# Kernel optimization log

Hardware: AMD Instinct MI355X
Metric: run time of the kernel (lower is better)

The kernel has to match this reference:

```python
import jax, jax.numpy as jnp
import numpy as np

TOP_N = 10
N_HEADS = 8

def _layernorm(x, g, b, eps=1e-5):
    mu = jnp.mean(x, axis=-1, keepdims=True)
    var = jnp.mean((x - mu) ** 2, axis=-1, keepdims=True)
    return (x - mu) * jax.lax.rsqrt(var + eps) * g + b

def setup_inputs() -> dict:
    key = jax.random.key(0)
    ks = jax.random.split(key, 16)
    B, N, D = 4096, 32768, 512
    s = 1.0 / np.sqrt(D)
    inp = {
        "visit_rep": jax.random.normal(ks[0], (B, D), jnp.float32),
        "E_mem_patient_rep": jax.random.normal(ks[1], (N, D), jnp.float32),
        "E_mem_med_rep": jax.random.normal(ks[2], (N, D), jnp.float32),
        "Wq": jax.random.uniform(ks[3], (D, D), jnp.float32, -s, s),
        "Wk": jax.random.uniform(ks[4], (D, D), jnp.float32, -s, s),
        "Wv": jax.random.uniform(ks[5], (D, D), jnp.float32, -s, s),
        "bq": jnp.zeros((D,), jnp.float32),
        "bk": jnp.zeros((D,), jnp.float32),
        "bv": jnp.zeros((D,), jnp.float32),
        "Wo": jax.random.uniform(ks[6], (D, D), jnp.float32, -s, s),
        "bo": jnp.zeros((D,), jnp.float32),
        "W1": jax.random.uniform(ks[7], (D, D), jnp.float32, -s, s),
        "b1": jax.random.uniform(ks[8], (D,), jnp.float32, -s, s),
        "W2": jax.random.uniform(ks[9], (D, D), jnp.float32, -s, s),
        "b2": jax.random.uniform(ks[10], (D,), jnp.float32, -s, s),
        "ln1_g": jnp.ones((D,), jnp.float32),
        "ln1_b": jnp.zeros((D,), jnp.float32),
        "ln2_g": jnp.ones((D,), jnp.float32),
        "ln2_b": jnp.zeros((D,), jnp.float32),
    }
    return inp

def reference(visit_rep, E_mem_patient_rep, E_mem_med_rep,
              Wq, bq, Wk, bk, Wv, bv, Wo, bo,
              W1, b1, W2, b2, ln1_g, ln1_b, ln2_g, ln2_b):
    B, D = visit_rep.shape
    H = N_HEADS
    hd = D // H
    # --- exact L2 kNN (faiss GpuIndexFlatL2 equivalent), detached ---
    q = jax.lax.stop_gradient(visit_rep)
    M = jax.lax.stop_gradient(E_mem_patient_rep)
    d2 = (jnp.sum(q * q, axis=1, keepdims=True)
          - 2.0 * q @ M.T
          + jnp.sum(M * M, axis=1)[None, :])          # [B, N]
    _, I = jax.lax.top_k(-d2, TOP_N)                    # [B, top_n]
    k = E_mem_patient_rep[I]                            # [B, top_n, D]
    v = E_mem_med_rep[I]                                # [B, top_n, D]
    # --- multihead attention, query seq-len 1 ---
    qh = (visit_rep @ Wq.T + bq).reshape(B, H, hd)
    kh = (k @ Wk.T + bk).reshape(B, TOP_N, H, hd)
    vh = (v @ Wv.T + bv).reshape(B, TOP_N, H, hd)
    scores = jnp.einsum("bhd,bnhd->bhn", qh, kh) / np.sqrt(hd)
    attn = jax.nn.softmax(scores, axis=-1)
    ctx = jnp.einsum("bhn,bnhd->bhd", attn, vh).reshape(B, D)
    attn_out = ctx @ Wo.T + bo
    # --- residual + norms + FFN (dropout = identity in eval) ---
    x = _layernorm(visit_rep + attn_out, ln1_g, ln1_b)
    ff = (jax.nn.leaky_relu(x @ W1.T + b1, 0.01)) @ W2.T + b2
    x = _layernorm(x + ff, ln2_g, ln2_b)
    return x
```

## Files before the change

kernel.cpp:

```cpp
#include <hip/hip_runtime.h>
#include <math.h>

#define BQ 4096
#define NMEM 32768
#define DD 512
#define TOPN 10
#define NBX 128
#define ENT 2048
#define NCF 16
#define LK 6
#define FINF 3.402823466e+38f
#define IMAX 0x7fffffff

typedef __attribute__((ext_vector_type(8))) short    bf16x8;
typedef __attribute__((ext_vector_type(4))) float    f32x4;
typedef __attribute__((ext_vector_type(4))) int      i32x4;

__device__ __forceinline__ unsigned short f2bf(float x) {
    unsigned int u = __float_as_uint(x);
    u += 0x7fffu + ((u >> 16) & 1u);
    return (unsigned short)(u >> 16);
}
__device__ __forceinline__ void async_copy16(const void* gp, void* lp) {
    __builtin_amdgcn_global_load_lds(
        (const __attribute__((address_space(1))) void*)gp,
        (__attribute__((address_space(3))) void*)lp, 16, 0, 0);
}
__device__ __forceinline__ bool lt_si(float s, int j, float s2, int j2) {
    return (s < s2) || (s == s2 && j < j2);
}
template<int KN>
__device__ __forceinline__ void topk_insert(float (&ts)[KN], int (&ti)[KN], float s, int j) {
    if (!lt_si(s, j, ts[KN-1], ti[KN-1])) return;
    #pragma unroll
    for (int p = KN-1; p > 0; --p) {
        if (lt_si(s, j, ts[p-1], ti[p-1])) { ts[p] = ts[p-1]; ti[p] = ti[p-1]; }
        else { ts[p] = s; ti[p] = j; return; }
    }
    ts[0] = s; ti[0] = j;
}

struct CastDesc {
    const float* in[7];
    unsigned short* out[7];
    int start[8];
};
__global__ __launch_bounds__(256) void cast_multi_kernel(CastDesc d) {
    int blk = blockIdx.x;
    int seg = 0;
    #pragma unroll
    for (int s = 0; s < 6; ++s) seg += (blk >= d.start[s + 1]) ? 1 : 0;
    int local = blk - d.start[seg];
    int i = (local * 256 + threadIdx.x) * 4;
    float4 v = *(const float4*)(d.in[seg] + i);
    ushort4 o;
    o.x = f2bf(v.x); o.y = f2bf(v.y); o.z = f2bf(v.z); o.w = f2bf(v.w);
    *(ushort4*)(d.out[seg] + i) = o;
}

__global__ __launch_bounds__(256) void cast_norm2_kernel(
        const float* __restrict__ inA, unsigned short* __restrict__ outA,
        const float* __restrict__ inB, unsigned short* __restrict__ outB,
        const float* __restrict__ inV,
        signed char* __restrict__ outA8, signed char* __restrict__ outV8,
        float* __restrict__ mnorm, float* __restrict__ msc,
        float* __restrict__ qsc) {
    const int pl = blockIdx.y;
    if (pl == 2 && blockIdx.x >= BQ / 4) return;
    const float* in = (pl == 0) ? inA : (pl == 1 ? inB : inV);
    int row = blockIdx.x * 4 + (threadIdx.x >> 6);
    int lane = threadIdx.x & 63;
    const float* r = in + (size_t)row * DD + lane * 8;
    float4 a = *(const float4*)r;
    float4 b = *(const float4*)(r + 4);
    if (pl < 2) {
        unsigned short* out = pl ? outB : outA;
        ushort4 oa, ob;
        oa.x = f2bf(a.x); oa.y = f2bf(a.y); oa.z = f2bf(a.z); oa.w = f2bf(a.w);
        ob.x = f2bf(b.x); ob.y = f2bf(b.y); ob.z = f2bf(b.z); ob.w = f2bf(b.w);
        unsigned short* op = out + (size_t)row * DD + lane * 8;
        *(ushort4*)op = oa; *(ushort4*)(op + 4) = ob;
    }
    if (pl != 1) {
        float ax = fmaxf(fmaxf(fmaxf(fabsf(a.x), fabsf(a.y)), fmaxf(fabsf(a.z), fabsf(a.w))),
                         fmaxf(fmaxf(fabsf(b.x), fabsf(b.y)), fmaxf(fabsf(b.z), fabsf(b.w))));
        float s = a.x*a.x + a.y*a.y + a.z*a.z + a.w*a.w
                + b.x*b.x + b.y*b.y + b.z*b.z + b.w*b.w;
        #pragma unroll
        for (int off = 32; off; off >>= 1) {
            ax = fmaxf(ax, __shfl_xor(ax, off, 64));
            if (pl == 0) s += __shfl_xor(s, off, 64);
        }
        ax = fmaxf(ax, 1e-30f);
        float inv = 127.0f / ax;
        int q[8];
        q[0] = __float2int_rn(a.x*inv); q[1] = __float2int_rn(a.y*inv);
        q[2] = __float2int_rn(a.z*inv); q[3] = __float2int_rn(a.w*inv);
        q[4] = __float2int_rn(b.x*inv); q[5] = __float2int_rn(b.y*inv);
        q[6] = __float2int_rn(b.z*inv); q[7] = __float2int_rn(b.w*inv);
        unsigned w0 = (q[0]&255) | ((q[1]&255)<<8) | ((q[2]&255)<<16) | ((unsigned)(q[3]&255)<<24);
        unsigned w1 = (q[4]&255) | ((q[5]&255)<<8) | ((q[6]&255)<<16) | ((unsigned)(q[7]&255)<<24);
        signed char* o8 = (pl == 0 ? outA8 : outV8) + (size_t)row * DD + lane * 8;
        *(uint2*)o8 = make_uint2(w0, w1);
        if (lane == 0) {
            if (pl == 0) { mnorm[row] = s; msc[row] = ax * (1.0f/127.0f); }
            else         { qsc[row] = ax * (1.0f/127.0f); }
        }
    }
}

__global__ __launch_bounds__(512, 4) void gemm_knn_kernel(
        const signed char* __restrict__ Q8,
        const signed char* __restrict__ M8,
        const float* __restrict__ mnorm, const float* __restrict__ msc,
        const float* __restrict__ qsc,
        unsigned* __restrict__ cand_part) {
    __shared__ __align__(16) union {
        struct { signed char A[2][128][64]; signed char B[2][256][64]; } g;
        unsigned S[64 * 133];
    } sh;
    __shared__ float qs[128];
    const int tid  = threadIdx.x;
    const int lane = tid & 63;
    const int wave = tid >> 6;
    const int quad = lane >> 4, c16 = lane & 15;
    const int wm = wave >> 2, wn = wave & 3;
    const int m0 = blockIdx.y * 128, n0 = blockIdx.x * 256;
    const int srow   = tid >> 2;
    const int schunk = (tid & 3) ^ ((tid >> 3) & 3);
    const signed char* ag = Q8 + (size_t)(m0 + srow) * DD + schunk * 16;
    const signed char* bg = M8 + (size_t)(n0 + srow) * DD + schunk * 16;
    const int cq = (quad ^ ((c16 >> 1) & 3)) * 16;

    i32x4 acc[4][4] = {};
    i32x4 af[4], bf[4];

    if (tid < 128) qs[tid] = qsc[m0 + tid];

#define STG(tt) do {                                                            \
    const int s_ = (tt) & 1;                                                    \
    async_copy16(ag + (size_t)(tt)*64,            &sh.g.A[s_][srow][(tid & 3) * 16]);      \
    async_copy16(bg + (size_t)(tt)*64,            &sh.g.B[s_][srow][(tid & 3) * 16]);      \
    async_copy16(bg + (size_t)(tt)*64 + 128*DD,   &sh.g.B[s_][128 + srow][(tid & 3) * 16]);\
} while (0)
#define RD(tt) do {                                                             \
    const int s_ = (tt) & 1;                                                    \
    _Pragma("unroll")                                                           \
    for (int mt = 0; mt < 4; ++mt)                                              \
        af[mt] = *(const i32x4*)&sh.g.A[s_][wm*64 + mt*16 + c16][cq];           \
    _Pragma("unroll")                                                           \
    for (int nt = 0; nt < 4; ++nt)                                              \
        bf[nt] = *(const i32x4*)&sh.g.B[s_][wn*64 + nt*16 + c16][cq];           \
} while (0)
#define MM() do {                                                               \
    _Pragma("unroll")                                                           \
    for (int mt = 0; mt < 4; ++mt)                                              \
        _Pragma("unroll")                                                       \
        for (int nt = 0; nt < 4; ++nt)                                          \
            acc[mt][nt] = __builtin_amdgcn_mfma_i32_16x16x64_i8(                \
                af[mt], bf[nt], acc[mt][nt], 0, 0, 0);                          \
} while (0)

    STG(0);
    asm volatile("s_waitcnt vmcnt(0)" ::: "memory");
    __builtin_amdgcn_s_barrier();
    __builtin_amdgcn_sched_barrier(0);

    #pragma unroll
    for (int t = 0; t < 8; ++t) {
        RD(t);
        if (t < 7) STG(t + 1);
        __builtin_amdgcn_sched_barrier(0);
        asm volatile("s_waitcnt lgkmcnt(0)" ::: "memory");
        __builtin_amdgcn_sched_barrier(0);
        __builtin_amdgcn_s_setprio(1);
        MM();
        __builtin_amdgcn_s_setprio(0);
        __builtin_amdgcn_sched_barrier(0);
        asm volatile("s_waitcnt vmcnt(0)" ::: "memory");
        __builtin_amdgcn_sched_barrier(0);
        __builtin_amdgcn_s_barrier();
    }
#undef STG
#undef RD
#undef MM

    float mn[4], ms2[4];
    #pragma unroll
    for (int nt = 0; nt < 4; ++nt) {
        int col = n0 + wn*64 + nt*16 + c16;
        mn[nt]  = mnorm[col];
        ms2[nt] = -2.0f * msc[col];
    }
    const int rrow = tid >> 2, rq = tid & 3;
    __syncthreads();
    #pragma unroll
    for (int p = 0; p < 4; ++p) {
        if (wn == p) {
            #pragma unroll
            for (int mt = 0; mt < 4; ++mt)
                #pragma unroll
                for (int nt = 0; nt < 4; ++nt) {
                    uint4 w;
                    #pragma unroll
                    for (int r = 0; r < 4; ++r) {
                        float coef = ms2[nt] * qs[wm*64 + mt*16 + quad*4 + r];
                        float s = fmaxf(fmaf(coef, (float)acc[mt][nt][r], mn[nt]), 0.f);
                        (&w.x)[r] = (__float_as_uint(s) & 0xFFFFFF80u)
                                  | (unsigned)((p & 1) * 64 + nt * 16 + c16);
                    }
                    *(uint4*)&sh.S[(nt*16 + c16) * 133 + wm*64 + mt*16 + quad*4] = w;
                }
        }
        __syncthreads();
        unsigned s0 = 0xFFFFFFFFu, s1 = 0xFFFFFFFFu, s2 = 0xFFFFFFFFu, s3 = 0xFFFFFFFFu;
        #pragma unroll
        for (int m = 0; m < 16; ++m) {
            unsigned nv = sh.S[(rq*16 + m) * 133 + rrow];
            unsigned lo;
            lo = min(s0, nv); nv = max(s0, nv); s0 = lo;
            lo = min(s1, nv); nv = max(s1, nv); s1 = lo;
            lo = min(s2, nv); nv = max(s2, nv); s2 = lo;
            lo = min(s3, nv); nv = max(s3, nv); s3 = lo;
        }
        unsigned p0 = (unsigned)__shfl_xor((int)s0, 1, 64);
        unsigned p1 = (unsigned)__shfl_xor((int)s1, 1, 64);
        unsigned p2 = (unsigned)__shfl_xor((int)s2, 1, 64);
        unsigned p3 = (unsigned)__shfl_xor((int)s3, 1, 64);
        unsigned b0 = min(s0, p3), b1 = min(s1, p2), b2 = min(s2, p1), b3 = min(s3, p0);
        unsigned t0 = min(b0, b2), t2 = max(b0, b2), t1 = min(b1, b3), t3 = max(b1, b3);
        s0 = min(t0, t1); s1 = max(t0, t1); s2 = min(t2, t3); s3 = max(t2, t3);
        p0 = (unsigned)__shfl_xor((int)s0, 2, 64);
        p1 = (unsigned)__shfl_xor((int)s1, 2, 64);
        p2 = (unsigned)__shfl_xor((int)s2, 2, 64);
        p3 = (unsigned)__shfl_xor((int)s3, 2, 64);
        b0 = min(s0, p3); b1 = min(s1, p2); b2 = min(s2, p1); b3 = min(s3, p0);
        if (rq == p) {
            *(uint4*)(cand_part + (size_t)(m0 + rrow) * ENT + blockIdx.x * 16 + p * 4) =
                make_uint4(b0, b1, b2, b3);
        }
        __syncthreads();
    }
}

__global__ __launch_bounds__(256) void knn_select_kernel(
        const unsigned* __restrict__ cand_part,
        const float* __restrict__ Q, const float* __restrict__ Mm,
        const float* __restrict__ mnorm,
        int* __restrict__ knn_idx) {
    const int row = blockIdx.x;
    const int wave = threadIdx.x >> 6, lane = threadIdx.x & 63;
    __shared__ unsigned sk[64];
    __shared__ int      sc[64];
    __shared__ int      ids[NCF];
    __shared__ float    d2s[NCF];

    unsigned ks[LK]; int ti[LK];
    #pragma unroll
    for (int q = 0; q < LK; ++q) { ks[q] = 0xFFFFFFFFu; ti[q] = IMAX; }
    const uint4* p4 = (const uint4*)(cand_part + (size_t)row * ENT) + wave * 128;
    #pragma unroll
    for (int i = 0; i < 2; ++i) {
        uint4 v = p4[lane + 64 * i];
        #pragma unroll
        for (int e = 0; e < 4; ++e) {
            unsigned k = (&v.x)[e];
            int pos = wave * 512 + (lane + 64 * i) * 4 + e;
            int gcol = (pos >> 3) * 128 + (int)(k & 127u);
            bool cm[LK];
            #pragma unroll
            for (int q = 0; q < LK; ++q) cm[q] = k < ks[q];
            #pragma unroll
            for (int q = LK - 1; q > 0; --q) {
                unsigned tns = cm[q] ? k : ks[q];  int tni = cm[q] ? gcol : ti[q];
                ks[q] = cm[q-1] ? ks[q-1] : tns;
                ti[q] = cm[q-1] ? ti[q-1] : tni;
            }
            ks[0] = cm[0] ? k : ks[0];
            ti[0] = cm[0] ? gcol : ti[0];
        }
    }
    #pragma unroll
    for (int r = 0; r < NCF; ++r) {
        unsigned mk = ks[0]; int mi = ti[0];
        #pragma unroll
        for (int off = 1; off < 64; off <<= 1) {
            unsigned ok = (unsigned)__shfl_xor((int)mk, off, 64);
            int      oi = __shfl_xor(mi, off, 64);
            bool t = (ok < mk) || (ok == mk && oi < mi);
            mk = t ? ok : mk; mi = t ? oi : mi;
        }
        bool win = (ks[0] == mk) && (ti[0] == mi);
        #pragma unroll
        for (int q = 0; q < LK - 1; ++q) {
            ks[q] = win ? ks[q+1] : ks[q];
            ti[q] = win ? ti[q+1] : ti[q];
        }
        ks[LK-1] = win ? 0xFFFFFFFFu : ks[LK-1];
        ti[LK-1] = win ? IMAX : ti[LK-1];
        if (lane == r) { sk[wave * NCF + r] = mk; sc[wave * NCF + r] = mi; }
    }
    __syncthreads();
    if (wave == 0) {
        unsigned myk = sk[lane];
        int      myc = sc[lane];
        #pragma unroll
        for (int r = 0; r < NCF; ++r) {
            unsigned mk = myk; int mi = myc;
            #pragma unroll
            for (int off = 1; off < 64; off <<= 1) {
                unsigned ok = (unsigned)__shfl_xor((int)mk, off, 64);
                int      oi = __shfl_xor(mi, off, 64);
                bool t = (ok < mk) || (ok == mk && oi < mi);
                mk = t ? ok : mk; mi = t ? oi : mi;
            }
            bool win = (myk == mk) && (myc == mi);
            myk = win ? 0xFFFFFFFFu : myk;
            myc = win ? IMAX : myc;
            if (lane == r) ids[r] = mi;
        }
    }
    __syncthreads();
    float4 q0 = *(const float4*)(Q + (size_t)row * DD + lane * 8);
    float4 q1 = *(const float4*)(Q + (size_t)row * DD + lane * 8 + 4);
    for (int c = wave; c < NCF; c += 4) {
        int j = ids[c];
        const float* mr = Mm + (size_t)j * DD;
        float4 m0 = *(const float4*)(mr + lane * 8);
        float4 m1 = *(const float4*)(mr + lane * 8 + 4);
        float dot = q0.x*m0.x + q0.y*m0.y + q0.z*m0.z + q0.w*m0.w
                  + q1.x*m1.x + q1.y*m1.y + q1.z*m1.z + q1.w*m1.w;
        #pragma unroll
        for (int off = 32; off; off >>= 1) dot += __shfl_xor(dot, off, 64);
        if (lane == 0) d2s[c] = fmaf(-2.f, dot, mnorm[j]);
    }
    __syncthreads();
    if (threadIdx.x == 0) {
        float ts[TOPN]; int tj[TOPN];
        #pragma unroll
        for (int p = 0; p < TOPN; ++p) { ts[p] = FINF; tj[p] = IMAX; }
        for (int c = 0; c < NCF; ++c) topk_insert<TOPN>(ts, tj, d2s[c], ids[c]);
        #pragma unroll
        for (int p = 0; p < TOPN; ++p) knn_idx[row * TOPN + p] = tj[p];
    }
}

template<int ACT, int OUT_BF16>
__global__ __launch_bounds__(256) void gemm_bf16_nt(
        const unsigned short* __restrict__ A,
        const unsigned short* __restrict__ B,
        const float* __restrict__ bias,
        void* __restrict__ Cout, int ldc) {
    __shared__ __align__(16) unsigned short As[128 * 64];
    __shared__ __align__(16) unsigned short Bs[128 * 64];
    const int tid  = threadIdx.x;
    const int wave = tid >> 6, lane = tid & 63;
    const int quad = lane >> 4, c16 = lane & 15;
    const int m0 = blockIdx.y * 128, n0 = blockIdx.x * 128;
    const int wm0 = (wave >> 1) * 64, wn0 = (wave & 1) * 64;
    const int srow = wave * 32 + (lane >> 3);
    const int schunk = (lane & 7) ^ ((lane >> 3) & 7);
    const int xsw = c16 & 7;

    f32x4 acc[4][4] = {};

    for (int kt = 0; kt < DD; kt += 64) {
        __syncthreads();
        #pragma unroll
        for (int i = 0; i < 4; ++i) {
            const unsigned short* ga = A + (size_t)(m0 + srow + i * 8) * DD + kt + schunk * 8;
            async_copy16(ga, &As[(wave * 32 + i * 8) * 64]);
            const unsigned short* gb = B + (size_t)(n0 + srow + i * 8) * DD + kt + schunk * 8;
            async_copy16(gb, &Bs[(wave * 32 + i * 8) * 64]);
        }
        __syncthreads();
        #pragma unroll
        for (int ks = 0; ks < 64; ks += 32) {
            const int coff = (((ks >> 3) + quad) ^ xsw) << 3;
            bf16x8 af[4], bff[4];
            #pragma unroll
            for (int mt = 0; mt < 4; ++mt)
                af[mt] = *(const bf16x8*)&As[(wm0 + mt * 16 + c16) * 64 + coff];
            #pragma unroll
            for (int nt = 0; nt < 4; ++nt)
                bff[nt] = *(const bf16x8*)&Bs[(wn0 + nt * 16 + c16) * 64 + coff];
            #pragma unroll
            for (int mt = 0; mt < 4; ++mt)
                #pragma unroll
                for (int nt = 0; nt < 4; ++nt)
                    acc[mt][nt] = __builtin_amdgcn_mfma_f32_16x16x32_bf16(
                        af[mt], bff[nt], acc[mt][nt], 0, 0, 0);
        }
    }
    #pragma unroll
    for (int nt = 0; nt < 4; ++nt) {
        int ncol = n0 + wn0 + nt * 16 + c16;
        float bv = bias[ncol];
        #pragma unroll
        for (int mt = 0; mt < 4; ++mt) {
            size_t rbase = (size_t)(m0 + wm0 + mt * 16 + quad * 4) * ldc + ncol;
            #pragma unroll
            for (int r = 0; r < 4; ++r) {
                float v = acc[mt][nt][r] + bv;
                if (ACT == 1) v = v >= 0.f ? v : 0.01f * v;
                if (OUT_BF16) ((unsigned short*)Cout)[rbase + (size_t)r * ldc] = f2bf(v);
                else          ((float*)Cout)[rbase + (size_t)r * ldc] = v;
            }
        }
    }
}

struct G3 {
    const unsigned short* A[3];
    const unsigned short* B[3];
    const float* bias[3];
    void* C[3];
    int obf[3];
};
__global__ __launch_bounds__(256) void gemm3_kernel(G3 g) {
    const int yy = blockIdx.y;
    const int z = (yy >= 512) ? 2 : (yy >= 256 ? 1 : 0);
    const int my = yy - z * 256;
    __shared__ __align__(16) unsigned short As[128 * 64];
    __shared__ __align__(16) unsigned short Bs[128 * 64];
    const unsigned short* A = g.A[z];
    const unsigned short* B = g.B[z];
    const int tid  = threadIdx.x;
    const int wave = tid >> 6, lane = tid & 63;
    const int quad = lane >> 4, c16 = lane & 15;
    const int m0 = my * 128, n0 = blockIdx.x * 128;
    const int wm0 = (wave >> 1) * 64, wn0 = (wave & 1) * 64;
    const int srow = wave * 32 + (lane >> 3);
    const int schunk = (lane & 7) ^ ((lane >> 3) & 7);
    const int xsw = c16 & 7;

    f32x4 acc[4][4] = {};

    for (int kt = 0; kt < DD; kt += 64) {
        __syncthreads();
        #pragma unroll
        for (int i = 0; i < 4; ++i) {
            const unsigned short* ga = A + (size_t)(m0 + srow + i * 8) * DD + kt + schunk * 8;
            async_copy16(ga, &As[(wave * 32 + i * 8) * 64]);
            const unsigned short* gb = B + (size_t)(n0 + srow + i * 8) * DD + kt + schunk * 8;
            async_copy16(gb, &Bs[(wave * 32 + i * 8) * 64]);
        }
        __syncthreads();
        #pragma unroll
        for (int ks = 0; ks < 64; ks += 32) {
            const int coff = (((ks >> 3) + quad) ^ xsw) << 3;
            bf16x8 af[4], bff[4];
            #pragma unroll
            for (int mt = 0; mt < 4; ++mt)
                af[mt] = *(const bf16x8*)&As[(wm0 + mt * 16 + c16) * 64 + coff];
            #pragma unroll
            for (int nt = 0; nt < 4; ++nt)
                bff[nt] = *(const bf16x8*)&Bs[(wn0 + nt * 16 + c16) * 64 + coff];
            #pragma unroll
            for (int mt = 0; mt < 4; ++mt)
                #pragma unroll
                for (int nt = 0; nt < 4; ++nt)
                    acc[mt][nt] = __builtin_amdgcn_mfma_f32_16x16x32_bf16(
                        af[mt], bff[nt], acc[mt][nt], 0, 0, 0);
        }
    }
    const int obf = g.obf[z];
    #pragma unroll
    for (int nt = 0; nt < 4; ++nt) {
        int ncol = n0 + wn0 + nt * 16 + c16;
        float bv = g.bias[z][ncol];
        #pragma unroll
        for (int mt = 0; mt < 4; ++mt) {
            size_t rbase = (size_t)(m0 + wm0 + mt * 16 + quad * 4) * DD + ncol;
            #pragma unroll
            for (int r = 0; r < 4; ++r) {
                float v = acc[mt][nt][r] + bv;
                if (obf) ((unsigned short*)g.C[z])[rbase + (size_t)r * DD] = f2bf(v);
                else     ((float*)g.C[z])[rbase + (size_t)r * DD] = v;
            }
        }
    }
}

__global__ __launch_bounds__(512) void attn_kernel(
        const float* __restrict__ qh, const unsigned short* __restrict__ Kall,
        const unsigned short* __restrict__ Vall, const int* __restrict__ knn_idx,
        unsigned short* __restrict__ ctx_b) {
    const int b = blockIdx.x;
    const int h = threadIdx.x >> 6;
    const int l = threadIdx.x & 63;
    const int col = (h << 6) + l;
    int idxs[TOPN];
    #pragma unroll
    for (int n = 0; n < TOPN; ++n) idxs[n] = knn_idx[b * TOPN + n];
    const float q = qh[(size_t)b * DD + col];
    float sc[TOPN];
    #pragma unroll
    for (int n = 0; n < TOPN; ++n) {
        float p = q * __uint_as_float((unsigned)Kall[(size_t)idxs[n] * DD + col] << 16);
        #pragma unroll
        for (int off = 32; off; off >>= 1) p += __shfl_xor(p, off, 64);
        sc[n] = p * 0.125f;
    }
    float mx = sc[0];
    #pragma unroll
    for (int n = 1; n < TOPN; ++n) mx = fmaxf(mx, sc[n]);
    float se = 0.f;
    #pragma unroll
    for (int n = 0; n < TOPN; ++n) { sc[n] = expf(sc[n] - mx); se += sc[n]; }
    const float inv = 1.f / se;
    float o = 0.f;
    #pragma unroll
    for (int n = 0; n < TOPN; ++n)
        o = fmaf(sc[n] * inv,
                 __uint_as_float((unsigned)Vall[(size_t)idxs[n] * DD + col] << 16), o);
    ctx_b[(size_t)b * DD + col] = f2bf(o);
}

template<int EMIT_BF16>
__global__ __launch_bounds__(256) void add_ln_kernel(
        const float* __restrict__ X, const float* __restrict__ Y,
        const float* __restrict__ g, const float* __restrict__ be,
        float* __restrict__ out, unsigned short* __restrict__ out_b) {
    const int row = blockIdx.x;
    const int t = threadIdx.x;
    const size_t base = (size_t)row * DD;
    float v0 = X[base + t]       + Y[base + t];
    float v1 = X[base + 256 + t] + Y[base + 256 + t];
    float s = v0 + v1, sq = v0 * v0 + v1 * v1;
    #pragma unroll
    for (int off = 32; off; off >>= 1) { s += __shfl_xor(s, off, 64); sq += __shfl_xor(sq, off, 64); }
    __shared__ float rs[4], rq[4];
    const int w = t >> 6, l = t & 63;
    if (l == 0) { rs[w] = s; rq[w] = sq; }
    __syncthreads();
    float tot  = rs[0] + rs[1] + rs[2] + rs[3];
    float totq = rq[0] + rq[1] + rq[2] + rq[3];
    float mu = tot * (1.f / DD);
    float var = totq * (1.f / DD) - mu * mu;
    float rstd = rsqrtf(var + 1e-5f);
    float o0 = (v0 - mu) * rstd * g[t]       + be[t];
    float o1 = (v1 - mu) * rstd * g[256 + t] + be[256 + t];
    out[base + t] = o0;
    out[base + 256 + t] = o1;
    if (EMIT_BF16) {
        out_b[base + t] = f2bf(o0);
        out_b[base + 256 + t] = f2bf(o1);
    }
}

extern "C" void kernel_launch(void* const* d_in, const int* in_sizes, int n_in,
                              void* d_out, int out_size, void* d_ws, size_t ws_size,
                              hipStream_t stream) {
    const float* visit = (const float*)d_in[0];
    const float* Epat  = (const float*)d_in[1];
    const float* Emed  = (const float*)d_in[2];
    const float* Wq = (const float*)d_in[3];
    const float* Wk = (const float*)d_in[4];
    const float* Wv = (const float*)d_in[5];
    const float* bq = (const float*)d_in[6];
    const float* bk = (const float*)d_in[7];
    const float* bv = (const float*)d_in[8];
    const float* Wo = (const float*)d_in[9];
    const float* bo = (const float*)d_in[10];
    const float* W1 = (const float*)d_in[11];
    const float* b1 = (const float*)d_in[12];
    const float* W2 = (const float*)d_in[13];
    const float* b2 = (const float*)d_in[14];
    const float* ln1g = (const float*)d_in[15];
    const float* ln1b = (const float*)d_in[16];
    const float* ln2g = (const float*)d_in[17];
    const float* ln2b = (const float*)d_in[18];
    float* out = (float*)d_out;

    char* base = (char*)d_ws;
    const size_t MB = 1u << 20;
    float* mnorm   = (float*)(base);
    float* msc     = (float*)(base + 256*1024);
    float* qsc     = (float*)(base + 512*1024);
    int*   knn_idx = (int*)  (base + 2*MB);
    float* qh      = (float*)(base + 3*MB);
    float* attn_o  = qh;
    float* x1      = (float*)(base + 11*MB);
    float* ff      = (float*)(base + 19*MB);
    unsigned short* Qb    = (unsigned short*)(base + 27*MB);
    unsigned short* ctx_b = (unsigned short*)(base + 31*MB);
    unsigned short* x1_b  = (unsigned short*)(base + 35*MB);
    unsigned short* h1_b  = (unsigned short*)(base + 39*MB);
    unsigned short* Wq_b  = (unsigned short*)(base + 43*MB);
    unsigned short* Wk_b  = Wq_b + 262144;
    unsigned short* Wv_b  = Wk_b + 262144;
    unsigned short* Wo_b  = Wv_b + 262144;
    unsigned short* W1_b  = Wo_b + 262144;
    unsigned short* W2_b  = W1_b + 262144;
    unsigned short* Mb     = (unsigned short*)(base + 46*MB);
    unsigned short* Emed_b = (unsigned short*)(base + 78*MB);
    unsigned short* Kall = (unsigned short*)(base + 110*MB);
    unsigned short* Vall = Kall + (size_t)NMEM * DD;
    unsigned* cand_part = (unsigned*)Kall;
    signed char* M8 = (signed char*)(base + 142*MB);
    signed char* Q8 = (signed char*)(base + 158*MB);

    cast_norm2_kernel<<<dim3(NMEM / 4, 3), 256, 0, stream>>>(
        Epat, Mb, Emed, Emed_b, visit, M8, Q8, mnorm, msc, qsc);
    CastDesc cd;
    cd.in[0] = visit; cd.out[0] = Qb;
    cd.in[1] = Wq; cd.in[2] = Wk; cd.in[3] = Wv; cd.in[4] = Wo; cd.in[5] = W1; cd.in[6] = W2;
    cd.out[1] = Wq_b; cd.out[2] = Wk_b; cd.out[3] = Wv_b; cd.out[4] = Wo_b; cd.out[5] = W1_b; cd.out[6] = W2_b;
    cd.start[0] = 0; cd.start[1] = 2048;
    for (int s = 2; s <= 7; ++s) cd.start[s] = cd.start[s-1] + 256;
    cast_multi_kernel<<<cd.start[7], 256, 0, stream>>>(cd);

    gemm_knn_kernel<<<dim3(NBX, BQ / 128), 512, 0, stream>>>(Q8, M8, mnorm, msc, qsc, cand_part);
    knn_select_kernel<<<BQ, 256, 0, stream>>>(cand_part, visit, Epat, mnorm, knn_idx);

    G3 g3;
    g3.A[0] = Mb;     g3.B[0] = Wk_b; g3.bias[0] = bk; g3.C[0] = Kall; g3.obf[0] = 1;
    g3.A[1] = Emed_b; g3.B[1] = Wv_b; g3.bias[1] = bv; g3.C[1] = Vall; g3.obf[1] = 1;
    g3.A[2] = Qb;     g3.B[2] = Wq_b; g3.bias[2] = bq; g3.C[2] = qh;   g3.obf[2] = 0;
    gemm3_kernel<<<dim3(4, 544), 256, 0, stream>>>(g3);

    attn_kernel<<<BQ, 512, 0, stream>>>(qh, Kall, Vall, knn_idx, ctx_b);

    gemm_bf16_nt<0,0><<<dim3(4, BQ / 128), 256, 0, stream>>>(ctx_b, Wo_b, bo, attn_o, DD);
    add_ln_kernel<1><<<BQ, 256, 0, stream>>>(visit, attn_o, ln1g, ln1b, x1, x1_b);
    gemm_bf16_nt<1,1><<<dim3(4, BQ / 128), 256, 0, stream>>>(x1_b, W1_b, b1, h1_b, DD);
    gemm_bf16_nt<0,0><<<dim3(4, BQ / 128), 256, 0, stream>>>(h1_b, W2_b, b2, ff,   DD);
    add_ln_kernel<0><<<BQ, 256, 0, stream>>>(x1, ff, ln2g, ln2b, out, nullptr);
}
```

Measured before the change: 536.1 us.

## Swap GEMM operand roles so top-k selection runs in registers without LDS transpose

The kNN GEMM now places memory rows on the MFMA M dimension and queries on N, with each block covering 256 memory rows and 128 queries. Each lane therefore holds distances for one query across several memory rows, so the per-query top-4 can be built with register sorting networks and cross-quad shuffles. This removes the LDS score transpose, its union buffer and the four barrier-separated selection passes. Norms and scales are staged into shared arrays, and the candidate index encoding changes to match the new tiling.

```diff
diff --git a/kernel.cpp b/kernel.cpp
--- a/kernel.cpp
+++ b/kernel.cpp
@@ -115,42 +115,44 @@
         const float* __restrict__ mnorm, const float* __restrict__ msc,
         const float* __restrict__ qsc,
         unsigned* __restrict__ cand_part) {
-    __shared__ __align__(16) union {
-        struct { signed char A[2][128][64]; signed char B[2][256][64]; } g;
-        unsigned S[64 * 133];
+    __shared__ __align__(16) struct {
+        signed char A[2][256][64];
+        signed char B[2][128][64];
     } sh;
-    __shared__ float qs[128];
+    __shared__ float tb_mn[256], tb_ms2[256], qsl[128];
     const int tid  = threadIdx.x;
     const int lane = tid & 63;
     const int wave = tid >> 6;
     const int quad = lane >> 4, c16 = lane & 15;
-    const int wm = wave >> 2, wn = wave & 3;
-    const int m0 = blockIdx.y * 128, n0 = blockIdx.x * 256;
+    const int wmem = wave >> 1, wq = wave & 1;
+    const int mb0 = blockIdx.x * 256;
+    const int q0  = blockIdx.y * 128;
     const int srow   = tid >> 2;
     const int schunk = (tid & 3) ^ ((tid >> 3) & 3);
-    const signed char* ag = Q8 + (size_t)(m0 + srow) * DD + schunk * 16;
-    const signed char* bg = M8 + (size_t)(n0 + srow) * DD + schunk * 16;
+    const signed char* ag = M8 + (size_t)(mb0 + srow) * DD + schunk * 16;
+    const signed char* bg = Q8 + (size_t)(q0 + srow) * DD + schunk * 16;
     const int cq = (quad ^ ((c16 >> 1) & 3)) * 16;
 
     i32x4 acc[4][4] = {};
     i32x4 af[4], bf[4];
 
-    if (tid < 128) qs[tid] = qsc[m0 + tid];
+    if (tid < 256)      { tb_mn[tid] = mnorm[mb0 + tid]; tb_ms2[tid] = -2.0f * msc[mb0 + tid]; }
+    else if (tid < 384) { qsl[tid - 256] = qsc[q0 + tid - 256]; }
 
 #define STG(tt) do {                                                            \
     const int s_ = (tt) & 1;                                                    \
-    async_copy16(ag + (size_t)(tt)*64,            &sh.g.A[s_][srow][(tid & 3) * 16]);      \
-    async_copy16(bg + (size_t)(tt)*64,            &sh.g.B[s_][srow][(tid & 3) * 16]);      \
-    async_copy16(bg + (size_t)(tt)*64 + 128*DD,   &sh.g.B[s_][128 + srow][(tid & 3) * 16]);\
+    async_copy16(ag + (size_t)(tt)*64,            &sh.A[s_][srow][(tid & 3) * 16]);      \
+    async_copy16(ag + (size_t)(tt)*64 + 128*DD,   &sh.A[s_][128 + srow][(tid & 3) * 16]);\
+    async_copy16(bg + (size_t)(tt)*64,            &sh.B[s_][srow][(tid & 3) * 16]);      \
 } while (0)
 #define RD(tt) do {                                                             \
     const int s_ = (tt) & 1;                                                    \
     _Pragma("unroll")                                                           \
     for (int mt = 0; mt < 4; ++mt)                                              \
-        af[mt] = *(const i32x4*)&sh.g.A[s_][wm*64 + mt*16 + c16][cq];           \
+        af[mt] = *(const i32x4*)&sh.A[s_][wmem*64 + mt*16 + c16][cq];           \
     _Pragma("unroll")                                                           \
     for (int nt = 0; nt < 4; ++nt)                                              \
-        bf[nt] = *(const i32x4*)&sh.g.B[s_][wn*64 + nt*16 + c16][cq];           \
+        bf[nt] = *(const i32x4*)&sh.B[s_][wq*64 + nt*16 + c16][cq];             \
 } while (0)
 #define MM() do {                                                               \
     _Pragma("unroll")                                                           \
@@ -185,61 +187,53 @@
 #undef RD
 #undef MM
 
-    float mn[4], ms2[4];
     #pragma unroll
     for (int nt = 0; nt < 4; ++nt) {
-        int col = n0 + wn*64 + nt*16 + c16;
-        mn[nt]  = mnorm[col];
-        ms2[nt] = -2.0f * msc[col];
-    }
-    const int rrow = tid >> 2, rq = tid & 3;
-    __syncthreads();
-    #pragma unroll
-    for (int p = 0; p < 4; ++p) {
-        if (wn == p) {
-            #pragma unroll
-            for (int mt = 0; mt < 4; ++mt)
+        float qv = qsl[wq*64 + nt*16 + c16];
+        unsigned s0, s1, s2, s3;
+        #pragma unroll
+        for (int mt = 0; mt < 4; ++mt) {
+            unsigned k0, k1, k2, k3, lo, hi;
+            {
+                unsigned kk[4];
                 #pragma unroll
-                for (int nt = 0; nt < 4; ++nt) {
-                    uint4 w;
-                    #pragma unroll
-                    for (int r = 0; r < 4; ++r) {
-                        float coef = ms2[nt] * qs[wm*64 + mt*16 + quad*4 + r];
-                        float s = fmaxf(fmaf(coef, (float)acc[mt][nt][r], mn[nt]), 0.f);
-                        (&w.x)[r] = (__float_as_uint(s) & 0xFFFFFF80u)
-                                  | (unsigned)((p & 1) * 64 + nt * 16 + c16);
-                    }
-                    *(uint4*)&sh.S[(nt*16 + c16) * 133 + wm*64 + mt*16 + quad*4] = w;
+                for (int r = 0; r < 4; ++r) {
+                    int mrow = wmem*64 + mt*16 + quad*4 + r;
+                    float s = fmaxf(fmaf(tb_ms2[mrow] * qv, (float)acc[mt][nt][r], tb_mn[mrow]), 0.f);
+                    kk[r] = (__float_as_uint(s) & 0xFFFFFF80u)
+                          | (unsigned)(((wmem & 1) << 6) | (mt*16 + quad*4 + r));
                 }
-        }
-        __syncthreads();
-        unsigned s0 = 0xFFFFFFFFu, s1 = 0xFFFFFFFFu, s2 = 0xFFFFFFFFu, s3 = 0xFFFFFFFFu;
-        #pragma unroll
-        for (int m = 0; m < 16; ++m) {
-            unsigned nv = sh.S[(rq*16 + m) * 133 + rrow];
-            unsigned lo;
-            lo = min(s0, nv); nv = max(s0, nv); s0 = lo;
-            lo = min(s1, nv); nv = max(s1, nv); s1 = lo;
-            lo = min(s2, nv); nv = max(s2, nv); s2 = lo;
-            lo = min(s3, nv); nv = max(s3, nv); s3 = lo;
-        }
-        unsigned p0 = (unsigned)__shfl_xor((int)s0, 1, 64);
-        unsigned p1 = (unsigned)__shfl_xor((int)s1, 1, 64);
-        unsigned p2 = (unsigned)__shfl_xor((int)s2, 1, 64);
-        unsigned p3 = (unsigned)__shfl_xor((int)s3, 1, 64);
-        unsigned b0 = min(s0, p3), b1 = min(s1, p2), b2 = min(s2, p1), b3 = min(s3, p0);
-        unsigned t0 = min(b0, b2), t2 = max(b0, b2), t1 = min(b1, b3), t3 = max(b1, b3);
-        s0 = min(t0, t1); s1 = max(t0, t1); s2 = min(t2, t3); s3 = max(t2, t3);
-        p0 = (unsigned)__shfl_xor((int)s0, 2, 64);
-        p1 = (unsigned)__shfl_xor((int)s1, 2, 64);
-        p2 = (unsigned)__shfl_xor((int)s2, 2, 64);
-        p3 = (unsigned)__shfl_xor((int)s3, 2, 64);
-        b0 = min(s0, p3); b1 = min(s1, p2); b2 = min(s2, p1); b3 = min(s3, p0);
-        if (rq == p) {
-            *(uint4*)(cand_part + (size_t)(m0 + rrow) * ENT + blockIdx.x * 16 + p * 4) =
-                make_uint4(b0, b1, b2, b3);
-        }
-        __syncthreads();
+                k0 = kk[0]; k1 = kk[1]; k2 = kk[2]; k3 = kk[3];
+            }
+            lo = min(k0,k1); hi = max(k0,k1); k0 = lo; k1 = hi;
+            lo = min(k2,k3); hi = max(k2,k3); k2 = lo; k3 = hi;
+            lo = min(k0,k2); hi = max(k0,k2); k0 = lo; k2 = hi;
+            lo = min(k1,k3); hi = max(k1,k3); k1 = lo; k3 = hi;
+            lo = min(k1,k2); hi = max(k1,k2); k1 = lo; k2 = hi;
+            if (mt == 0) { s0 = k0; s1 = k1; s2 = k2; s3 = k3; }
+            else {
+                unsigned b0 = min(s0,k3), b1 = min(s1,k2), b2 = min(s2,k1), b3 = min(s3,k0);
+                unsigned t0 = min(b0,b2), t2 = max(b0,b2), t1 = min(b1,b3), t3 = max(b1,b3);
+                s0 = min(t0,t1); s1 = max(t0,t1); s2 = min(t2,t3); s3 = max(t2,t3);
+            }
+        }
+        unsigned p0, p1, p2, p3, b0, b1, b2, b3, t0, t1, t2, t3;
+        p0 = (unsigned)__shfl_xor((int)s0, 16, 64);
+        p1 = (unsigned)__shfl_xor((int)s1, 16, 64);
+        p2 = (unsigned)__shfl_xor((int)s2, 16, 64);
+        p3 = (unsigned)__shfl_xor((int)s3, 16, 64);
+        b0 = min(s0,p3); b1 = min(s1,p2); b2 = min(s2,p1); b3 = min(s3,p0);
+        t0 = min(b0,b2); t2 = max(b0,b2); t1 = min(b1,b3); t3 = max(b1,b3);
+        s0 = min(t0,t1); s1 = max(t0,t1); s2 = min(t2,t3); s3 = max(t2,t3);
+        p0 = (unsigned)__shfl_xor((int)s0, 32, 64);
+        p1 = (unsigned)__shfl_xor((int)s1, 32, 64);
+        p2 = (unsigned)__shfl_xor((int)s2, 32, 64);
+        p3 = (unsigned)__shfl_xor((int)s3, 32, 64);
+        b0 = min(s0,p3); b1 = min(s1,p2); b2 = min(s2,p1); b3 = min(s3,p0);
+        if (quad == 0) {
+            *(uint4*)(cand_part + (size_t)(q0 + wq*64 + nt*16 + c16) * ENT
+                      + blockIdx.x * 16 + wmem * 4) = make_uint4(b0, b1, b2, b3);
+        }
     }
 }
 
```

New measurement: 495.3 us. 1.08x faster.
